# Kernel tuning notes

Measured on AMD Instinct MI355X. Metric: run time of the kernel, lower is better.

The kernel has to match this reference:

```python
import jax, jax.numpy as jnp
import numpy as np

STRIDE = 1
PADDING = 1

def setup_inputs() -> dict:
    key = jax.random.key(0)
    k1, k2, k3 = jax.random.split(key, 3)
    N, C_in, H, W = 32, 128, 56, 56
    C_out, K = 256, 3
    inputs = jax.random.normal(k1, (N, C_in, H, W), dtype=jnp.float32)
    # trunc_normal(std=0.1) approximated by clipped normal
    filters = jnp.clip(jax.random.normal(k2, (C_out, C_in, K, K), dtype=jnp.float32) * 0.1, -0.2, 0.2)
    bias = jnp.clip(jax.random.normal(k3, (C_out,), dtype=jnp.float32) * 0.1, -0.2, 0.2)
    return {"inputs": inputs, "filters": filters, "bias": bias}

def reference(inputs, filters, bias):
    # Equivalent of the quadruple-loop conv: standard cross-correlation,
    # NCHW input, OIHW filters, stride/padding from module config.
    out = jax.lax.conv_general_dilated(
        inputs, filters,
        window_strides=(STRIDE, STRIDE),
        padding=[(PADDING, PADDING), (PADDING, PADDING)],
        dimension_numbers=("NCHW", "OIHW", "NCHW"),
    )
    out = out + bias[None, :, None, None]
    return out
```

## Files before the change

kernel.cpp:

```cpp
#include <hip/hip_runtime.h>

#define CIN    128
#define HH     56
#define WW_    56
#define NBATCH 32
#define COUT   256
#define KTOT   1152
#define PLANE  3136
#define HP     58
#define BM     128
#define BN     128
#define NSTEP  36

#define WB_OFF   0
#define XP_OFF   (1u << 20)

#define SLOT_BYTES 16384
#define LDS_BYTES  (4 * SLOT_BYTES)

typedef __attribute__((ext_vector_type(8))) short bf16x8;
typedef __attribute__((ext_vector_type(4))) float f32x4;

__device__ __forceinline__ unsigned short f2bf(float f) {
    unsigned int u = __builtin_bit_cast(unsigned int, f);
    u += 0x7fffu + ((u >> 16) & 1u);
    return (unsigned short)(u >> 16);
}

__device__ __forceinline__ void gl_lds16(const void* g, void* l) {
    __builtin_amdgcn_global_load_lds(
        (const __attribute__((address_space(1))) void*)g,
        (__attribute__((address_space(3))) void*)l, 16, 0, 0);
}

__global__ __launch_bounds__(256)
void wprep(const float* __restrict__ w, unsigned short* __restrict__ wb) {
    __shared__ __align__(16) unsigned short L[KTOT];
    const int o = blockIdx.x;
    const int t = threadIdx.x;
    const float4* src = (const float4*)(w + (size_t)o * KTOT);
    #pragma unroll
    for (int e = 0; e < 2; ++e) {
        const int q = t + e * 256;
        if (q < 288) {
            const float4 v = src[q];
            #pragma unroll
            for (int u = 0; u < 4; ++u) {
                const int idx = q * 4 + u;
                const int ci  = idx / 9;
                const int tap = idx - ci * 9;
                L[tap * 128 + ci] = f2bf(((const float*)&v)[u]);
            }
        }
    }
    __syncthreads();
    if (t < 144)
        ((uint4*)(wb + (size_t)o * KTOT))[t] = ((const uint4*)L)[t];
}

__global__ __launch_bounds__(256)
void xprep(const float* __restrict__ in, unsigned short* __restrict__ xp) {
    const int b  = blockIdx.x;
    const int n  = b / HP;
    const int ho = b - n * HP;
    const int t  = threadIdx.x;
    uint4* orow = (uint4*)(xp + (((size_t)n * HP + ho) * HP) * CIN);

    if (ho == 0 || ho == HP - 1) {
        #pragma unroll
        for (int e = 0; e < 4; ++e) {
            const int idx = t + e * 256;
            if (idx < 928) orow[idx] = (uint4){0u, 0u, 0u, 0u};
        }
        return;
    }

    __shared__ unsigned short L[CIN * 57];
    const int h  = ho - 1;
    const int w  = t & 63;
    const int cb = t >> 6;
    if (w < WW_) {
        const float* ib = in + ((size_t)n * CIN) * PLANE + (size_t)h * WW_ + w;
        #pragma unroll
        for (int e = 0; e < 32; ++e) {
            const int ci = cb * 32 + e;
            L[ci * 57 + w] = f2bf(ib[(size_t)ci * PLANE]);
        }
    }
    __syncthreads();

    #pragma unroll
    for (int e = 0; e < 4; ++e) {
        const int idx = t + e * 256;
        if (idx < 928) {
            const int wo = idx >> 4;
            const int ch = idx & 15;
            uint4 pk = {0u, 0u, 0u, 0u};
            if (wo >= 1 && wo <= WW_) {
                const int wi = wo - 1;
                unsigned v[8];
                #pragma unroll
                for (int i = 0; i < 8; ++i)
                    v[i] = L[(ch * 8 + i) * 57 + wi];
                pk.x = v[0] | (v[1] << 16);
                pk.y = v[2] | (v[3] << 16);
                pk.z = v[4] | (v[5] << 16);
                pk.w = v[6] | (v[7] << 16);
            }
            orow[idx] = pk;
        }
    }
}

__global__ __launch_bounds__(256, 2)
void conv_mfma(const unsigned short* __restrict__ wb,
               const unsigned short* __restrict__ xp,
               const float* __restrict__ bias,
               float* __restrict__ out)
{
    extern __shared__ __align__(16) char lds[];

    const int t = threadIdx.x;

    const int bid0 = blockIdx.x;
    const int bid  = (bid0 & 7) * ((NBATCH * PLANE / BN * 2) >> 3) + (bid0 >> 3);
    const int c0   = (bid & 1) * BM;
    const int pix0 = (bid >> 1) * BN;

    const char* aSrc[2]; const char* bSrc[2];
    int aDst[2], bDst[2];
    #pragma unroll
    for (int e = 0; e < 2; ++e) {
        const int idx  = t + e * 256;
        const int line = idx >> 3;
        const int us   = (idx & 7) ^ (line & 7);
        const int row  = 2 * line + (us >> 2);
        const int koff = (us & 3) * 16;
        aSrc[e] = (const char*)wb + (size_t)(c0 + row) * (KTOT * 2) + koff;
        const int pix = pix0 + row;
        const int n   = pix / PLANE;
        const int rem = pix - n * PLANE;
        const int h   = rem / WW_;
        const int w   = rem - h * WW_;
        bSrc[e] = (const char*)xp + ((size_t)(n * HP + h) * HP + w) * (CIN * 2) + koff;
        aDst[e] = idx * 16;
        bDst[e] = 8192 + idx * 16;
    }

    auto stage = [&](int hi) {
        char* slot = lds + (hi & 3) * SLOT_BYTES;
        const int tap  = hi >> 2;
        const int q    = hi & 3;
        const int aoff = tap * 256 + q * 64;
        const int boff = ((tap / 3) * HP + (tap % 3)) * (CIN * 2) + q * 64;
        gl_lds16(aSrc[0] + aoff, slot + aDst[0]);
        gl_lds16(aSrc[1] + aoff, slot + aDst[1]);
        gl_lds16(bSrc[0] + boff, slot + bDst[0]);
        gl_lds16(bSrc[1] + boff, slot + bDst[1]);
    };

    const int lane = t & 63;
    const int wave = t >> 6;
    const int wm   = (wave & 1) * 64;
    const int wn   = (wave >> 1) * 64;
    const int lr   = lane & 15;
    const int quad = lane >> 4;
    int offA[4], offB[4];
    #pragma unroll
    for (int i = 0; i < 4; ++i) {
        const int ra = wm + i * 16 + lr;
        offA[i] = (ra >> 1) * 128 + ((((ra & 1) * 4 + quad) ^ ((ra >> 1) & 7)) * 16);
        const int rb = wn + i * 16 + lr;
        offB[i] = 8192 + (rb >> 1) * 128 + ((((rb & 1) * 4 + quad) ^ ((rb >> 1) & 7)) * 16);
    }

    auto ldreg = [&](int hi, bf16x8 (&fr)[8]) {
        const char* slot = lds + (hi & 3) * SLOT_BYTES;
        #pragma unroll
        for (int i = 0; i < 4; ++i) fr[i]     = *(const bf16x8*)(slot + offA[i]);
        #pragma unroll
        for (int i = 0; i < 4; ++i) fr[4 + i] = *(const bf16x8*)(slot + offB[i]);
    };

    f32x4 acc[4][4];
    #pragma unroll
    for (int i = 0; i < 4; ++i)
        #pragma unroll
        for (int j = 0; j < 4; ++j)
            acc[i][j] = (f32x4){0.f, 0.f, 0.f, 0.f};

    auto domfma = [&](bf16x8 (&fr)[8]) {
        __builtin_amdgcn_s_setprio(1);
        #pragma unroll
        for (int i = 0; i < 4; ++i)
            #pragma unroll
            for (int j = 0; j < 4; ++j)
                acc[i][j] = __builtin_amdgcn_mfma_f32_16x16x32_bf16(fr[i], fr[4 + j], acc[i][j], 0, 0, 0);
        __builtin_amdgcn_s_setprio(0);
    };

    auto step = [&](int hi, bf16x8 (&cur)[8], bf16x8 (&nxt)[8]) {
        asm volatile("s_waitcnt vmcnt(4)" ::: "memory");
        __builtin_amdgcn_s_barrier();
        asm volatile("s_waitcnt lgkmcnt(0)" ::: "memory");
        __builtin_amdgcn_sched_barrier(0);
        ldreg(hi + 1, nxt);
        if (hi + 3 < NSTEP) stage(hi + 3);
        domfma(cur);
    };

    stage(0); stage(1); stage(2);
    asm volatile("s_waitcnt vmcnt(8)" ::: "memory");
    __builtin_amdgcn_s_barrier();

    bf16x8 fA[8], fB[8];
    ldreg(0, fA);

    for (int h2 = 0; h2 < NSTEP - 2; h2 += 2) {
        step(h2,     fA, fB);
        step(h2 + 1, fB, fA);
    }
    asm volatile("s_waitcnt vmcnt(0)" ::: "memory");
    __builtin_amdgcn_s_barrier();
    asm volatile("s_waitcnt lgkmcnt(0)" ::: "memory");
    __builtin_amdgcn_sched_barrier(0);
    ldreg(35, fB);
    domfma(fA);
    asm volatile("s_waitcnt lgkmcnt(0)" ::: "memory");
    __builtin_amdgcn_sched_barrier(0);
    domfma(fB);

    #pragma unroll
    for (int j = 0; j < 4; ++j) {
        const int pg    = pix0 + wn + j * 16 + lr;
        const int ni    = pg / PLANE;
        const int inner = pg - ni * PLANE;
        float* op = out + (size_t)ni * (COUT * PLANE) + inner;
        #pragma unroll
        for (int i = 0; i < 4; ++i) {
            const int crow = c0 + wm + i * 16 + quad * 4;
            #pragma unroll
            for (int r = 0; r < 4; ++r)
                op[(size_t)(crow + r) * PLANE] = acc[i][j][r] + bias[crow + r];
        }
    }
}

extern "C" void kernel_launch(void* const* d_in, const int* in_sizes, int n_in,
                              void* d_out, int out_size, void* d_ws, size_t ws_size,
                              hipStream_t stream) {
    const float* in   = (const float*)d_in[0];
    const float* wt   = (const float*)d_in[1];
    const float* bias = (const float*)d_in[2];
    float* out        = (float*)d_out;

    unsigned short* wbuf = (unsigned short*)((char*)d_ws + WB_OFF);
    unsigned short* xpb  = (unsigned short*)((char*)d_ws + XP_OFF);

    (void)hipFuncSetAttribute((const void*)conv_mfma,
                              hipFuncAttributeMaxDynamicSharedMemorySize, LDS_BYTES);

    wprep<<<COUT, 256, 0, stream>>>(wt, wbuf);
    xprep<<<NBATCH * HP, 256, 0, stream>>>(in, xpb);

    conv_mfma<<<dim3((NBATCH * PLANE / BN) * 2), 256, LDS_BYTES, stream>>>(wbuf, xpb, bias, out);
}
```

Before: 212.7 us.

## Stage only weights in LDS, load activation fragments directly to registers

The conv kernel now stages only the weight tile through LDS in a 4-slot ring. Each wave loads its own activation (B) fragments straight from global memory into registers, one step ahead. Waves now split only along pixels (32 each), each covering all 128 output channels, and LDS per block is halved so occupancy can rise to 3 blocks per CU. The change trades LDS traffic and footprint for more global/L2 loads of activations, which are no longer shared across waves, and it adds exposed global-load latency on the B operand.

```diff
diff --git a/kernel.cpp b/kernel.cpp
--- a/kernel.cpp
+++ b/kernel.cpp
@@ -15,8 +15,7 @@
 #define WB_OFF   0
 #define XP_OFF   (1u << 20)
 
-#define SLOT_BYTES 16384
-#define LDS_BYTES  (4 * SLOT_BYTES)
+#define SLOT 8192
 
 typedef __attribute__((ext_vector_type(8))) short bf16x8;
 typedef __attribute__((ext_vector_type(4))) float f32x4;
@@ -112,13 +111,13 @@
     }
 }
 
-__global__ __launch_bounds__(256, 2)
+__global__ __launch_bounds__(256, 3)
 void conv_mfma(const unsigned short* __restrict__ wb,
                const unsigned short* __restrict__ xp,
                const float* __restrict__ bias,
                float* __restrict__ out)
 {
-    extern __shared__ __align__(16) char lds[];
+    __shared__ __align__(16) char lds[4 * SLOT];
 
     const int t = threadIdx.x;
 
@@ -127,118 +126,100 @@
     const int c0   = (bid & 1) * BM;
     const int pix0 = (bid >> 1) * BN;
 
-    const char* aSrc[2]; const char* bSrc[2];
-    int aDst[2], bDst[2];
+    const char* aSrc[2];
+    int aDst[2];
     #pragma unroll
     for (int e = 0; e < 2; ++e) {
-        const int idx  = t + e * 256;
-        const int line = idx >> 3;
-        const int us   = (idx & 7) ^ (line & 7);
-        const int row  = 2 * line + (us >> 2);
-        const int koff = (us & 3) * 16;
-        aSrc[e] = (const char*)wb + (size_t)(c0 + row) * (KTOT * 2) + koff;
-        const int pix = pix0 + row;
+        const int idx = t + e * 256;
+        const int row = idx >> 2;
+        const int lc  = (idx & 3) ^ ((idx >> 3) & 3);
+        aSrc[e] = (const char*)wb + (size_t)(c0 + row) * (KTOT * 2) + lc * 16;
+        aDst[e] = idx * 16;
+    }
+
+    auto stageA = [&](int hi) {
+        char* sl = lds + (hi & 3) * SLOT;
+        gl_lds16(aSrc[0] + hi * 64, sl + aDst[0]);
+        gl_lds16(aSrc[1] + hi * 64, sl + aDst[1]);
+    };
+
+    const int lane = t & 63;
+    const int wave = t >> 6;
+    const int wn   = wave * 32;
+    const int lr   = lane & 15;
+    const int quad = lane >> 4;
+    const char* bB[2];
+    #pragma unroll
+    for (int j = 0; j < 2; ++j) {
+        const int pix = pix0 + wn + j * 16 + lr;
         const int n   = pix / PLANE;
         const int rem = pix - n * PLANE;
         const int h   = rem / WW_;
         const int w   = rem - h * WW_;
-        bSrc[e] = (const char*)xp + ((size_t)(n * HP + h) * HP + w) * (CIN * 2) + koff;
-        aDst[e] = idx * 16;
-        bDst[e] = 8192 + idx * 16;
-    }
-
-    auto stage = [&](int hi) {
-        char* slot = lds + (hi & 3) * SLOT_BYTES;
+        bB[j] = (const char*)xp + ((size_t)(n * HP + h) * HP + w) * (CIN * 2) + quad * 16;
+    }
+
+    auto loadB = [&](int hi, bf16x8 (&bf)[2]) {
         const int tap  = hi >> 2;
-        const int q    = hi & 3;
-        const int aoff = tap * 256 + q * 64;
-        const int boff = ((tap / 3) * HP + (tap % 3)) * (CIN * 2) + q * 64;
-        gl_lds16(aSrc[0] + aoff, slot + aDst[0]);
-        gl_lds16(aSrc[1] + aoff, slot + aDst[1]);
-        gl_lds16(bSrc[0] + boff, slot + bDst[0]);
-        gl_lds16(bSrc[1] + boff, slot + bDst[1]);
+        const int boff = ((tap / 3) * HP + (tap % 3)) * (CIN * 2) + (hi & 3) * 64;
+        bf[0] = *(const bf16x8*)(bB[0] + boff);
+        bf[1] = *(const bf16x8*)(bB[1] + boff);
     };
 
-    const int lane = t & 63;
-    const int wave = t >> 6;
-    const int wm   = (wave & 1) * 64;
-    const int wn   = (wave >> 1) * 64;
-    const int lr   = lane & 15;
-    const int quad = lane >> 4;
-    int offA[4], offB[4];
-    #pragma unroll
-    for (int i = 0; i < 4; ++i) {
-        const int ra = wm + i * 16 + lr;
-        offA[i] = (ra >> 1) * 128 + ((((ra & 1) * 4 + quad) ^ ((ra >> 1) & 7)) * 16);
-        const int rb = wn + i * 16 + lr;
-        offB[i] = 8192 + (rb >> 1) * 128 + ((((rb & 1) * 4 + quad) ^ ((rb >> 1) & 7)) * 16);
-    }
-
-    auto ldreg = [&](int hi, bf16x8 (&fr)[8]) {
-        const char* slot = lds + (hi & 3) * SLOT_BYTES;
-        #pragma unroll
-        for (int i = 0; i < 4; ++i) fr[i]     = *(const bf16x8*)(slot + offA[i]);
-        #pragma unroll
-        for (int i = 0; i < 4; ++i) fr[4 + i] = *(const bf16x8*)(slot + offB[i]);
-    };
-
-    f32x4 acc[4][4];
-    #pragma unroll
-    for (int i = 0; i < 4; ++i)
-        #pragma unroll
-        for (int j = 0; j < 4; ++j)
+    const int s = (lr >> 1) & 3;
+    int offA[8];
+    #pragma unroll
+    for (int i = 0; i < 8; ++i) {
+        const int row = i * 16 + lr;
+        offA[i] = row * 64 + ((quad ^ s) * 16);
+    }
+
+    f32x4 acc[8][2];
+    #pragma unroll
+    for (int i = 0; i < 8; ++i)
+        #pragma unroll
+        for (int j = 0; j < 2; ++j)
             acc[i][j] = (f32x4){0.f, 0.f, 0.f, 0.f};
 
-    auto domfma = [&](bf16x8 (&fr)[8]) {
+    auto step = [&](int hi, bf16x8 (&cur)[2], bf16x8 (&nxt)[2]) {
+        if (hi + 2 < NSTEP) asm volatile("s_waitcnt vmcnt(2)" ::: "memory");
+        else                asm volatile("s_waitcnt vmcnt(0)" ::: "memory");
+        __builtin_amdgcn_s_barrier();
+        const char* sl = lds + (hi & 3) * SLOT;
+        bf16x8 afr[8];
+        #pragma unroll
+        for (int i = 0; i < 8; ++i)
+            afr[i] = *(const bf16x8*)(sl + offA[i]);
+        if (hi + 1 < NSTEP) loadB(hi + 1, nxt);
+        if (hi + 3 < NSTEP) stageA(hi + 3);
         __builtin_amdgcn_s_setprio(1);
         #pragma unroll
-        for (int i = 0; i < 4; ++i)
+        for (int i = 0; i < 8; ++i)
             #pragma unroll
-            for (int j = 0; j < 4; ++j)
-                acc[i][j] = __builtin_amdgcn_mfma_f32_16x16x32_bf16(fr[i], fr[4 + j], acc[i][j], 0, 0, 0);
+            for (int j = 0; j < 2; ++j)
+                acc[i][j] = __builtin_amdgcn_mfma_f32_16x16x32_bf16(afr[i], cur[j], acc[i][j], 0, 0, 0);
         __builtin_amdgcn_s_setprio(0);
     };
 
-    auto step = [&](int hi, bf16x8 (&cur)[8], bf16x8 (&nxt)[8]) {
-        asm volatile("s_waitcnt vmcnt(4)" ::: "memory");
-        __builtin_amdgcn_s_barrier();
-        asm volatile("s_waitcnt lgkmcnt(0)" ::: "memory");
-        __builtin_amdgcn_sched_barrier(0);
-        ldreg(hi + 1, nxt);
-        if (hi + 3 < NSTEP) stage(hi + 3);
-        domfma(cur);
-    };
-
-    stage(0); stage(1); stage(2);
-    asm volatile("s_waitcnt vmcnt(8)" ::: "memory");
-    __builtin_amdgcn_s_barrier();
-
-    bf16x8 fA[8], fB[8];
-    ldreg(0, fA);
-
-    for (int h2 = 0; h2 < NSTEP - 2; h2 += 2) {
-        step(h2,     fA, fB);
-        step(h2 + 1, fB, fA);
-    }
-    asm volatile("s_waitcnt vmcnt(0)" ::: "memory");
-    __builtin_amdgcn_s_barrier();
-    asm volatile("s_waitcnt lgkmcnt(0)" ::: "memory");
-    __builtin_amdgcn_sched_barrier(0);
-    ldreg(35, fB);
-    domfma(fA);
-    asm volatile("s_waitcnt lgkmcnt(0)" ::: "memory");
-    __builtin_amdgcn_sched_barrier(0);
-    domfma(fB);
-
-    #pragma unroll
-    for (int j = 0; j < 4; ++j) {
+    bf16x8 b0[2], b1[2];
+    stageA(0); stageA(1);
+    loadB(0, b0);
+    stageA(2);
+
+    for (int h2 = 0; h2 < NSTEP; h2 += 2) {
+        step(h2,     b0, b1);
+        step(h2 + 1, b1, b0);
+    }
+
+    #pragma unroll
+    for (int j = 0; j < 2; ++j) {
         const int pg    = pix0 + wn + j * 16 + lr;
         const int ni    = pg / PLANE;
         const int inner = pg - ni * PLANE;
         float* op = out + (size_t)ni * (COUT * PLANE) + inner;
         #pragma unroll
-        for (int i = 0; i < 4; ++i) {
-            const int crow = c0 + wm + i * 16 + quad * 4;
+        for (int i = 0; i < 8; ++i) {
+            const int crow = c0 + i * 16 + quad * 4;
             #pragma unroll
             for (int r = 0; r < 4; ++r)
                 op[(size_t)(crow + r) * PLANE] = acc[i][j][r] + bias[crow + r];
@@ -257,11 +238,8 @@
     unsigned short* wbuf = (unsigned short*)((char*)d_ws + WB_OFF);
     unsigned short* xpb  = (unsigned short*)((char*)d_ws + XP_OFF);
 
-    (void)hipFuncSetAttribute((const void*)conv_mfma,
-                              hipFuncAttributeMaxDynamicSharedMemorySize, LDS_BYTES);
-
     wprep<<<COUT, 256, 0, stream>>>(wt, wbuf);
     xprep<<<NBATCH * HP, 256, 0, stream>>>(in, xpb);
 
-    conv_mfma<<<dim3((NBATCH * PLANE / BN) * 2), 256, LDS_BYTES, stream>>>(wbuf, xpb, bias, out);
-}
+    conv_mfma<<<dim3((NBATCH * PLANE / BN) * 2), 256, 0, stream>>>(wbuf, xpb, bias, out);
+}
```

Measured after the change: 230.8 us. 1.09x slower.
